# Kernel tuning notes

Hardware: AMD Instinct MI355X
Metric: run time of the kernel (lower is better)

## Reference

```python
import jax, jax.numpy as jnp
import numpy as np

EMBED_DIM = 1024
NUM_HEADS = 16
HEAD_DIM = EMBED_DIM // NUM_HEADS
BATCH = 2
SEQ = 2048


def setup_inputs() -> dict:
    key = jax.random.key(0)
    k_x, k_wi, k_bi, k_wo, k_bo = jax.random.split(key, 5)
    scale_in = 1.0 / np.sqrt(EMBED_DIM)
    x = jax.random.normal(k_x, (BATCH, SEQ, EMBED_DIM), dtype=jnp.float32)
    # nn.Linear stores weight [out, in]; we keep [in, out] for x @ W.
    w_in = jax.random.uniform(k_wi, (EMBED_DIM, 3 * EMBED_DIM), jnp.float32, -scale_in, scale_in)
    b_in = jax.random.uniform(k_bi, (3 * EMBED_DIM,), jnp.float32, -scale_in, scale_in)
    w_out = jax.random.uniform(k_wo, (EMBED_DIM, EMBED_DIM), jnp.float32, -scale_in, scale_in)
    b_out = jax.random.uniform(k_bo, (EMBED_DIM,), jnp.float32, -scale_in, scale_in)
    return {"x": x, "w_in": w_in, "b_in": b_in, "w_out": w_out, "b_out": b_out}


def reference(x, w_in, b_in, w_out, b_out):
    B, S, E = x.shape
    H, D = NUM_HEADS, HEAD_DIM
    inp = x @ w_in + b_in                       # [B,S,3E]
    que, key, val = jnp.split(inp, 3, axis=-1)  # each [B,S,E]
    que = que.reshape(B, S, H, D)
    key = key.reshape(B, S, H, D)
    val = val.reshape(B, S, H, D)
    scores = jnp.einsum('bshd,brhd->bhsr', que, key) * (1.0 / np.sqrt(D))
    weights = jax.nn.softmax(scores, axis=-1)   # [B,H,S,S]
    attn = jnp.einsum('bhsr,brhd->bshd', weights, val).reshape(B, S, E)
    return attn @ w_out + b_out
```

## Files before the change

### kernel.cpp

```cpp
#include <hip/hip_runtime.h>


typedef __bf16 bf16x8 __attribute__((ext_vector_type(8)));
typedef float  f32x4  __attribute__((ext_vector_type(4)));
typedef float  f32x16 __attribute__((ext_vector_type(16)));
typedef short  s16x8  __attribute__((ext_vector_type(8)));

__device__ __forceinline__ unsigned short f2b(float f) {
  unsigned u = __float_as_uint(f);
  unsigned r = u + 0x7fffu + ((u >> 16) & 1u);
  return (unsigned short)(r >> 16);
}

__device__ __forceinline__ unsigned cvt_pk_bf16(float a, float b) {
#if defined(__HIP_DEVICE_COMPILE__)
  unsigned r;
  asm("v_cvt_pk_bf16_f32 %0, %1, %2" : "=v"(r) : "v"(a), "v"(b));
  return r;
#else
  return (unsigned)f2b(a) | ((unsigned)f2b(b) << 16);
#endif
}

__device__ __forceinline__ void permlane32_swap(unsigned& a, unsigned& b) {
#if defined(__HIP_DEVICE_COMPILE__)
  asm("v_permlane32_swap_b32 %0, %1" : "+v"(a), "+v"(b));
#endif
}

__device__ __forceinline__ void gl_lds16(const void* g, void* l) {
  __builtin_amdgcn_global_load_lds(
      (__attribute__((address_space(1))) void*)g,
      (__attribute__((address_space(3))) void*)l, 16, 0, 0);
}

__device__ __forceinline__ void transpose_cast_body(
    const float* __restrict__ in, unsigned short* __restrict__ out,
    int R, int C, int bx, int by, int tid, float tile[64][65]) {
  int r0 = by * 64, c0 = bx * 64;
#pragma unroll
  for (int p = 0; p < 4; p++) {
    int i = tid + p * 256;
    int ri = i >> 4, c4 = (i & 15) * 4;
    float4 v = *(const float4*)&in[(size_t)(r0 + ri) * C + c0 + c4];
    tile[ri][c4 + 0] = v.x; tile[ri][c4 + 1] = v.y;
    tile[ri][c4 + 2] = v.z; tile[ri][c4 + 3] = v.w;
  }
  __syncthreads();
#pragma unroll
  for (int p = 0; p < 8; p++) {
    int i = tid + p * 256;
    int ci = i >> 5, rp = (i & 31) * 2;
    ushort2 o;
    o.x = f2b(tile[rp][ci]);
    o.y = f2b(tile[rp + 1][ci]);
    *(ushort2*)&out[(size_t)(c0 + ci) * R + r0 + rp] = o;
  }
}

__global__ __launch_bounds__(256) void prep_kernel(
    const float* __restrict__ x, unsigned short* __restrict__ xb,
    const float* __restrict__ w_in, unsigned short* __restrict__ wint,
    const float* __restrict__ w_out, unsigned short* __restrict__ woutt) {
  __shared__ float tile[64][65];
  int bid = blockIdx.x, tid = threadIdx.x;
  if (bid < 4096) {
    int i = bid * 256 + tid;
    float4 v = ((const float4*)x)[i];
    ushort4 o;
    o.x = f2b(v.x); o.y = f2b(v.y); o.z = f2b(v.z); o.w = f2b(v.w);
    ((ushort4*)xb)[i] = o;
  } else if (bid < 4864) {
    int l = bid - 4096;
    transpose_cast_body(w_in, wint, 1024, 3072, l % 48, l / 48, tid, tile);
  } else {
    int l = bid - 4864;
    transpose_cast_body(w_out, woutt, 1024, 1024, l % 16, l / 16, tid, tile);
  }
}

__global__ __launch_bounds__(256) void gemm_bt1(
    const unsigned short* __restrict__ A, const unsigned short* __restrict__ Bt,
    const float* __restrict__ bias, unsigned short* __restrict__ Cp,
    unsigned short* __restrict__ vtp,
    int M, int N, int K, int qcols, float qscale) {
  __shared__ __align__(16) unsigned short As[2][128 * 32];
  __shared__ __align__(16) unsigned short Bs[2][128 * 32];
  int tid = threadIdx.x;
  int wave = tid >> 6, lane = tid & 63;
  int m_l = lane & 15, quad = lane >> 4;
  int wm = (wave >> 1) * 64, wn = (wave & 1) * 64;
  int row = tid >> 2, kp = (tid & 3) << 3;
  const unsigned short* ag = A + (size_t)(blockIdx.y * 128 + row) * K + kp;
  const unsigned short* bg = Bt + (size_t)(blockIdx.x * 128 + row) * K + kp;
  f32x4 acc[4][4] = {};

  auto stage = [&](int k0, int s) {
    gl_lds16(ag + k0, &As[s][wave * 512]);
    gl_lds16(ag + (size_t)64 * K + k0, &As[s][2048 + wave * 512]);
    gl_lds16(bg + k0, &Bs[s][wave * 512]);
    gl_lds16(bg + (size_t)64 * K + k0, &Bs[s][2048 + wave * 512]);
  };
  auto compute = [&](int s) {
    bf16x8 af[4], bf[4];
#pragma unroll
    for (int i = 0; i < 4; i++)
      af[i] = *(const bf16x8*)&As[s][(wm + i * 16 + m_l) * 32 + quad * 8];
#pragma unroll
    for (int j = 0; j < 4; j++)
      bf[j] = *(const bf16x8*)&Bs[s][(wn + j * 16 + m_l) * 32 + quad * 8];
#pragma unroll
    for (int i = 0; i < 4; i++)
#pragma unroll
      for (int j = 0; j < 4; j++)
        acc[i][j] = __builtin_amdgcn_mfma_f32_16x16x32_bf16(af[i], bf[j], acc[i][j], 0, 0, 0);
  };

  stage(0, 0);
  __syncthreads();
  for (int k0 = 0; k0 < K; k0 += 64) {
    if (k0 + 32 < K) stage(k0 + 32, 1);
    compute(0);
    __syncthreads();
    if (k0 + 64 < K) stage(k0 + 64, 0);
    compute(1);
    __syncthreads();
  }

  float bv[4];
#pragma unroll
  for (int j = 0; j < 4; j++) bv[j] = bias[blockIdx.x * 128 + wn + j * 16 + m_l];
  bool isV = (blockIdx.x >= 16);
  int bb = (blockIdx.y * 128) >> 11;
  unsigned short* vbase = vtp + (size_t)bb * 16 * 64 * 2048;
#pragma unroll
  for (int i = 0; i < 4; i++) {
    int m = blockIdx.y * 128 + wm + i * 16 + quad * 4;
    int s = m & 2047;
#pragma unroll
    for (int j = 0; j < 4; j++) {
      int n = blockIdx.x * 128 + wn + j * 16 + m_l;
      float sc = (n < qcols) ? qscale : 1.0f;
      int nv = n - 2048;
#pragma unroll
      for (int r = 0; r < 4; r++) {
        float v = (acc[i][j][r] + bv[j]) * sc;
        unsigned short hv = f2b(v);
        Cp[(size_t)(m + r) * N + n] = hv;
        if (isV) vbase[(size_t)nv * 2048 + s + r] = hv;
      }
    }
  }
}

__global__ __launch_bounds__(512) void gemm_bt2(
    const unsigned short* __restrict__ A, const unsigned short* __restrict__ Bt,
    const float* __restrict__ bias, float* __restrict__ Cp, int M, int N, int K) {
  __shared__ __align__(16) unsigned short As[2][128 * 32];
  __shared__ __align__(16) unsigned short Bs[2][128 * 32];
  int tid = threadIdx.x;
  int wave = tid >> 6, lane = tid & 63;
  int m_l = lane & 15, quad = lane >> 4;
  int wm = (wave >> 2) * 64, wn = (wave & 3) * 32;
  int row = tid >> 2, kp = (tid & 3) << 3;
  const unsigned short* ag = A + (size_t)(blockIdx.y * 128 + row) * K + kp;
  const unsigned short* bg = Bt + (size_t)(blockIdx.x * 128 + row) * K + kp;
  f32x4 acc[4][2] = {};

  auto stage = [&](int k0, int s) {
    gl_lds16(ag + k0, &As[s][wave * 512]);
    gl_lds16(bg + k0, &Bs[s][wave * 512]);
  };
  auto compute = [&](int s) {
    bf16x8 af[4], bf[2];
#pragma unroll
    for (int i = 0; i < 4; i++)
      af[i] = *(const bf16x8*)&As[s][(wm + i * 16 + m_l) * 32 + quad * 8];
#pragma unroll
    for (int j = 0; j < 2; j++)
      bf[j] = *(const bf16x8*)&Bs[s][(wn + j * 16 + m_l) * 32 + quad * 8];
#pragma unroll
    for (int i = 0; i < 4; i++)
#pragma unroll
      for (int j = 0; j < 2; j++)
        acc[i][j] = __builtin_amdgcn_mfma_f32_16x16x32_bf16(af[i], bf[j], acc[i][j], 0, 0, 0);
  };

  stage(0, 0);
  __syncthreads();
  for (int k0 = 0; k0 < K; k0 += 64) {
    if (k0 + 32 < K) stage(k0 + 32, 1);
    compute(0);
    __syncthreads();
    if (k0 + 64 < K) stage(k0 + 64, 0);
    compute(1);
    __syncthreads();
  }

  float bv[2];
#pragma unroll
  for (int j = 0; j < 2; j++) bv[j] = bias[blockIdx.x * 128 + wn + j * 16 + m_l];
#pragma unroll
  for (int i = 0; i < 4; i++) {
    int m = blockIdx.y * 128 + wm + i * 16 + quad * 4;
#pragma unroll
    for (int j = 0; j < 2; j++) {
      int n = blockIdx.x * 128 + wn + j * 16 + m_l;
#pragma unroll
      for (int r = 0; r < 4; r++)
        Cp[(size_t)(m + r) * N + n] = acc[i][j][r] + bv[j];
    }
  }
}

__global__ __launch_bounds__(512, 4) void attn_kernel(
    const unsigned short* __restrict__ qkv, const unsigned short* __restrict__ vt,
    unsigned short* __restrict__ aout) {
  __shared__ __align__(16) unsigned short smem[40960];
  unsigned short* Qs  = smem;
  unsigned short* Ks0 = smem + 8192;
  unsigned short* Ks1 = smem + 16384;
  unsigned short* Vt0 = smem + 24576;
  unsigned short* Vt1 = smem + 32768;

  int bid = blockIdx.x;
  int qt = bid & 15, h = (bid >> 4) & 15, b = bid >> 8;
  int tid = threadIdx.x, wave = tid >> 6, lane = tid & 63;
  int l31 = lane & 31, hi = lane >> 5, l7 = lane & 7;
  int w03 = wave & 3;
  int koff = (wave >> 2) * 64;
  int q0 = qt * 128;
  const unsigned short* qb = qkv + (size_t)b * 2048 * 3072 + h * 64;
  const unsigned short* kb = qb + 1024;
  const unsigned short* vtb = vt + (size_t)(b * 16 + h) * 64 * 2048;

  int srow = tid >> 3;
  int sd0 = ((tid & 7) ^ (srow & 7)) * 8;
  int dv = tid >> 4;
  int sv = tid & 15;
  int gv = (sv & 8) | ((sv & 7) ^ (dv & 7));

  auto stageKV = [&](unsigned short* Kb, unsigned short* Vb, int kt) {
    gl_lds16(kb + (size_t)(kt + srow) * 3072 + sd0, Kb + wave * 512);
    gl_lds16(kb + (size_t)(kt + 64 + srow) * 3072 + sd0, Kb + 4096 + wave * 512);
    gl_lds16(vtb + (size_t)dv * 2048 + kt + gv * 8, Vb + wave * 512);
    gl_lds16(vtb + (size_t)(32 + dv) * 2048 + kt + gv * 8, Vb + 4096 + wave * 512);
  };

#pragma unroll
  for (int p = 0; p < 2; p++)
    gl_lds16(qb + (size_t)(q0 + p * 64 + srow) * 3072 + sd0, Qs + p * 4096 + wave * 512);
  stageKV(Ks0, Vt0, 0);
  __syncthreads();

  bf16x8 qf[4];
  int qrow = (w03 * 32 + l31) * 64;
#pragma unroll
  for (int ks = 0; ks < 4; ks++)
    qf[ks] = *(const bf16x8*)&Qs[qrow + ((2 * ks + hi) ^ l7) * 8];

  union { s16x8 s; bf16x8 v; } onesu;
  onesu.s = (s16x8){0x3F80, 0x3F80, 0x3F80, 0x3F80, 0x3F80, 0x3F80, 0x3F80, 0x3F80};

  f32x16 oacc[2] = {};
  f32x16 lacc = {};
  f32x16 z16 = {};

  auto computeKV = [&](const unsigned short* Kb, const unsigned short* Vb) {
#pragma unroll
    for (int tt = 0; tt < 2; tt++) {
      bf16x8 kf0 = *(const bf16x8*)&Kb[(koff + tt * 32 + l31) * 64 + ((2 * 0 + hi) ^ l7) * 8];
      f32x16 sacc = __builtin_amdgcn_mfma_f32_32x32x16_bf16(kf0, qf[0], z16, 0, 0, 0);
#pragma unroll
      for (int ks = 1; ks < 4; ks++) {
        bf16x8 kf = *(const bf16x8*)&Kb[(koff + tt * 32 + l31) * 64 + ((2 * ks + hi) ^ l7) * 8];
        sacc = __builtin_amdgcn_mfma_f32_32x32x16_bf16(kf, qf[ks], sacc, 0, 0, 0);
      }
      float pv[16];
#pragma unroll
      for (int i = 0; i < 16; i++) pv[i] = __builtin_exp2f(sacc[i]);
#pragma unroll
      for (int g = 0; g < 2; g++) {
        unsigned a0 = cvt_pk_bf16(pv[8 * g + 0], pv[8 * g + 1]);
        unsigned a1 = cvt_pk_bf16(pv[8 * g + 2], pv[8 * g + 3]);
        unsigned b0 = cvt_pk_bf16(pv[8 * g + 4], pv[8 * g + 5]);
        unsigned b1 = cvt_pk_bf16(pv[8 * g + 6], pv[8 * g + 7]);
        permlane32_swap(a0, b0);
        permlane32_swap(a1, b1);
        union { unsigned u[4]; bf16x8 v; } pf;
        pf.u[0] = a0; pf.u[1] = a1; pf.u[2] = b0; pf.u[3] = b1;
        lacc = __builtin_amdgcn_mfma_f32_32x32x16_bf16(onesu.v, pf.v, lacc, 0, 0, 0);
        int kc = tt * 2 + g;
#pragma unroll
        for (int dt = 0; dt < 2; dt++) {
          bf16x8 vf = *(const bf16x8*)&Vb[(dt * 32 + l31) * 128 +
                                          ((koff >> 3) | ((kc * 2 + hi) ^ l7)) * 8];
          oacc[dt] = __builtin_amdgcn_mfma_f32_32x32x16_bf16(vf, pf.v, oacc[dt], 0, 0, 0);
        }
      }
    }
  };

  for (int kt = 0; kt < 2048; kt += 256) {
    stageKV(Ks1, Vt1, kt + 128);
    __builtin_amdgcn_s_setprio(1);
    computeKV(Ks0, Vt0);
    __builtin_amdgcn_s_setprio(0);
    __syncthreads();
    if (kt + 256 < 2048) stageKV(Ks0, Vt0, kt + 256);
    __builtin_amdgcn_s_setprio(1);
    computeKV(Ks1, Vt1);
    __builtin_amdgcn_s_setprio(0);
    __syncthreads();
  }

  float* red = (float*)smem;
  float* lpred = red + 8192;
  if (wave >= 4) {
    float* basep = red + w03 * 2048;
#pragma unroll
    for (int dt = 0; dt < 2; dt++)
#pragma unroll
      for (int r = 0; r < 4; r++) {
        f32x4 c4 = {oacc[dt][4 * r + 0], oacc[dt][4 * r + 1],
                    oacc[dt][4 * r + 2], oacc[dt][4 * r + 3]};
        ((f32x4*)basep)[lane * 8 + ((dt * 4 + r) ^ (lane & 7))] = c4;
      }
    lpred[w03 * 64 + lane] = lacc[0];
  }
  __syncthreads();
  if (wave < 4) {
    float* basep = red + w03 * 2048;
#pragma unroll
    for (int dt = 0; dt < 2; dt++)
#pragma unroll
      for (int r = 0; r < 4; r++) {
        f32x4 c4 = ((f32x4*)basep)[lane * 8 + ((dt * 4 + r) ^ (lane & 7))];
        oacc[dt][4 * r + 0] += c4[0];
        oacc[dt][4 * r + 1] += c4[1];
        oacc[dt][4 * r + 2] += c4[2];
        oacc[dt][4 * r + 3] += c4[3];
      }
    float rl = 1.0f / (lacc[0] + lpred[w03 * 64 + lane]);

    unsigned short* ob = aout + (size_t)(b * 2048 + q0 + w03 * 32 + l31) * 1024 + h * 64;
#pragma unroll
    for (int dt = 0; dt < 2; dt++)
#pragma unroll
      for (int rq = 0; rq < 4; rq++) {
        union { uint2 u; ushort4 w; } pk;
        pk.u.x = cvt_pk_bf16(oacc[dt][4 * rq + 0] * rl, oacc[dt][4 * rq + 1] * rl);
        pk.u.y = cvt_pk_bf16(oacc[dt][4 * rq + 2] * rl, oacc[dt][4 * rq + 3] * rl);
        *(ushort4*)&ob[dt * 32 + rq * 8 + hi * 4] = pk.w;
      }
  }
}

extern "C" void kernel_launch(void* const* d_in, const int* in_sizes, int n_in,
                              void* d_out, int out_size, void* d_ws, size_t ws_size,
                              hipStream_t stream) {
  (void)in_sizes; (void)n_in; (void)out_size; (void)ws_size;
  const float* x     = (const float*)d_in[0];
  const float* w_in  = (const float*)d_in[1];
  const float* b_in  = (const float*)d_in[2];
  const float* w_out = (const float*)d_in[3];
  const float* b_out = (const float*)d_in[4];
  char* ws = (char*)d_ws;
  unsigned short* xb    = (unsigned short*)(ws + 0);
  unsigned short* wint  = (unsigned short*)(ws + 8388608);
  unsigned short* woutt = (unsigned short*)(ws + 14680064);
  unsigned short* qkv   = (unsigned short*)(ws + 16777216);
  unsigned short* vt    = (unsigned short*)(ws + 41943040);
  unsigned short* attn  = (unsigned short*)(ws + 50331648);
  float* out = (float*)d_out;

  const float QSCALE = 0.125f * 1.44269504088896f;

  prep_kernel<<<5120, 256, 0, stream>>>(x, xb, w_in, wint, w_out, woutt);
  gemm_bt1<<<dim3(24, 32), 256, 0, stream>>>(xb, wint, b_in, qkv, vt,
                                             4096, 3072, 1024, 1024, QSCALE);
  attn_kernel<<<512, 512, 0, stream>>>(qkv, vt, attn);
  gemm_bt2<<<dim3(8, 32), 512, 0, stream>>>(attn, woutt, b_out, out, 4096, 1024, 1024);
}
```

Before: 194.2 us.

## Triple-buffer GEMM LDS staging with explicit vmcnt waits

Both projection GEMMs move from a double-buffered LDS pipeline to a three-stage ring buffer. Loads for step k+2 are issued before computing step k, and completion is tracked with explicit s_waitcnt vmcnt counts plus raw s_barrier instead of __syncthreads. This keeps more global-to-LDS transfers in flight and needs one barrier pair per 32-wide K step rather than a full drain. It costs 50% more shared memory per block, which may reduce occupancy, and the hand-counted vmcnt values must match the number of outstanding loads.

```diff
diff --git a/kernel.cpp b/kernel.cpp
--- a/kernel.cpp
+++ b/kernel.cpp
@@ -33,6 +33,8 @@
       (__attribute__((address_space(1))) void*)g,
       (__attribute__((address_space(3))) void*)l, 16, 0, 0);
 }
+
+#define VMCNT(n) asm volatile("s_waitcnt vmcnt(" #n ")" ::: "memory")
 
 __device__ __forceinline__ void transpose_cast_body(
     const float* __restrict__ in, unsigned short* __restrict__ out,
@@ -84,8 +86,8 @@
     const float* __restrict__ bias, unsigned short* __restrict__ Cp,
     unsigned short* __restrict__ vtp,
     int M, int N, int K, int qcols, float qscale) {
-  __shared__ __align__(16) unsigned short As[2][128 * 32];
-  __shared__ __align__(16) unsigned short Bs[2][128 * 32];
+  __shared__ __align__(16) unsigned short As[3][128 * 32];
+  __shared__ __align__(16) unsigned short Bs[3][128 * 32];
   int tid = threadIdx.x;
   int wave = tid >> 6, lane = tid & 63;
   int m_l = lane & 15, quad = lane >> 4;
@@ -117,15 +119,25 @@
   };
 
   stage(0, 0);
-  __syncthreads();
-  for (int k0 = 0; k0 < K; k0 += 64) {
-    if (k0 + 32 < K) stage(k0 + 32, 1);
-    compute(0);
-    __syncthreads();
-    if (k0 + 64 < K) stage(k0 + 64, 0);
-    compute(1);
-    __syncthreads();
-  }
+  stage(32, 1);
+  int buf = 0;
+  for (int k0 = 0; k0 + 64 < K; k0 += 32) {
+    int pre = buf + 2; if (pre >= 3) pre -= 3;
+    stage(k0 + 64, pre);
+    VMCNT(8);
+    __builtin_amdgcn_s_barrier();
+    compute(buf);
+    __builtin_amdgcn_s_barrier();
+    buf = (buf + 1 == 3) ? 0 : buf + 1;
+  }
+  VMCNT(4);
+  __builtin_amdgcn_s_barrier();
+  compute(buf);
+  __builtin_amdgcn_s_barrier();
+  buf = (buf + 1 == 3) ? 0 : buf + 1;
+  VMCNT(0);
+  __builtin_amdgcn_s_barrier();
+  compute(buf);
 
   float bv[4];
 #pragma unroll
@@ -156,8 +168,8 @@
 __global__ __launch_bounds__(512) void gemm_bt2(
     const unsigned short* __restrict__ A, const unsigned short* __restrict__ Bt,
     const float* __restrict__ bias, float* __restrict__ Cp, int M, int N, int K) {
-  __shared__ __align__(16) unsigned short As[2][128 * 32];
-  __shared__ __align__(16) unsigned short Bs[2][128 * 32];
+  __shared__ __align__(16) unsigned short As[3][128 * 32];
+  __shared__ __align__(16) unsigned short Bs[3][128 * 32];
   int tid = threadIdx.x;
   int wave = tid >> 6, lane = tid & 63;
   int m_l = lane & 15, quad = lane >> 4;
@@ -187,15 +199,25 @@
   };
 
   stage(0, 0);
-  __syncthreads();
-  for (int k0 = 0; k0 < K; k0 += 64) {
-    if (k0 + 32 < K) stage(k0 + 32, 1);
-    compute(0);
-    __syncthreads();
-    if (k0 + 64 < K) stage(k0 + 64, 0);
-    compute(1);
-    __syncthreads();
-  }
+  stage(32, 1);
+  int buf = 0;
+  for (int k0 = 0; k0 + 64 < K; k0 += 32) {
+    int pre = buf + 2; if (pre >= 3) pre -= 3;
+    stage(k0 + 64, pre);
+    VMCNT(4);
+    __builtin_amdgcn_s_barrier();
+    compute(buf);
+    __builtin_amdgcn_s_barrier();
+    buf = (buf + 1 == 3) ? 0 : buf + 1;
+  }
+  VMCNT(2);
+  __builtin_amdgcn_s_barrier();
+  compute(buf);
+  __builtin_amdgcn_s_barrier();
+  buf = (buf + 1 == 3) ? 0 : buf + 1;
+  VMCNT(0);
+  __builtin_amdgcn_s_barrier();
+  compute(buf);
 
   float bv[2];
 #pragma unroll
```

Result: no change. 197.8 us (+1.9%).
